# Optimization experiments

Hardware: AMD Instinct MI355X
Metric: run time of the kernel (lower is better)

## Reference

```python
import jax, jax.numpy as jnp
import numpy as np

IMG = 512.0
B, C, A, H, W, M = 16, 3, 9, 128, 128, 32
K = 5 + C
N = A * H * W


def make_anchors():
    # SSD-style anchor grid: 3 scales x 3 aspect ratios per cell on a HxW grid.
    stride = IMG / H
    cx, cy = jnp.meshgrid(
        (jnp.arange(W, dtype=jnp.float32) + 0.5) * stride,
        (jnp.arange(H, dtype=jnp.float32) + 0.5) * stride,
        indexing='xy')
    scales = jnp.array([16.0, 32.0, 64.0], dtype=jnp.float32)
    ratios = jnp.array([0.5, 1.0, 2.0], dtype=jnp.float32)
    ws = (scales[:, None] * jnp.sqrt(ratios)[None, :]).reshape(-1)  # [A]
    hs = (scales[:, None] / jnp.sqrt(ratios)[None, :]).reshape(-1)
    cx = cx[:, :, None]; cy = cy[:, :, None]  # [H,W,1]
    x1 = cx - ws * 0.5; y1 = cy - hs * 0.5
    x2 = cx + ws * 0.5; y2 = cy + hs * 0.5
    anc = jnp.stack([x1, y1, x2, y2], axis=-1)  # [H,W,A,4]
    return anc.reshape(-1, 4)


def setup_inputs() -> dict:
    key = jax.random.key(0)
    k1, k2, k3, k4 = jax.random.split(key, 4)
    pred = jax.random.normal(k1, (B, A * K, H, W), dtype=jnp.float32)
    anchors = make_anchors()  # [N,4]
    xy = jax.random.uniform(k2, (B, M, 2), minval=0.0, maxval=IMG * 0.8)
    wh = jax.random.uniform(k3, (B, M, 2), minval=16.0, maxval=IMG * 0.2)
    gt_boxes = jnp.concatenate([xy, xy + wh], axis=-1).astype(jnp.float32)
    gt_labels = jax.random.randint(k4, (B, M), 1, C + 1).astype(jnp.int32)
    return {'pred': pred, 'anchors': anchors, 'gt_boxes': gt_boxes, 'gt_labels': gt_labels}


def iou_matrix(anc, boxes):
    # anc [N,4], boxes [M,4] -> [N,M]
    lt = jnp.maximum(anc[:, None, :2], boxes[None, :, :2])
    rb = jnp.minimum(anc[:, None, 2:], boxes[None, :, 2:])
    wh = jnp.clip(rb - lt, 0.0)
    inter = wh[..., 0] * wh[..., 1]
    area_a = (anc[:, 2] - anc[:, 0]) * (anc[:, 3] - anc[:, 1])
    area_b = (boxes[:, 2] - boxes[:, 0]) * (boxes[:, 3] - boxes[:, 1])
    union = area_a[:, None] + area_b[None, :] - inter
    return inter / jnp.maximum(union, 1e-9)


def encode_boxes(anc, boxes):
    ax = (anc[..., 0] + anc[..., 2]) * 0.5
    ay = (anc[..., 1] + anc[..., 3]) * 0.5
    aw = jnp.maximum(anc[..., 2] - anc[..., 0], 1e-6)
    ah = jnp.maximum(anc[..., 3] - anc[..., 1], 1e-6)
    gx = (boxes[..., 0] + boxes[..., 2]) * 0.5
    gy = (boxes[..., 1] + boxes[..., 3]) * 0.5
    gw = jnp.maximum(boxes[..., 2] - boxes[..., 0], 1e-6)
    gh = jnp.maximum(boxes[..., 3] - boxes[..., 1], 1e-6)
    return jnp.stack([(gx - ax) / aw, (gy - ay) / ah,
                      jnp.log(gw / aw), jnp.log(gh / ah)], axis=-1)


def bce_logits(x, t):
    return jnp.maximum(x, 0.0) - x * t + jnp.log1p(jnp.exp(-jnp.abs(x)))


def smooth_l1(d):
    ad = jnp.abs(d)
    return jnp.where(ad < 1.0, 0.5 * d * d, ad - 0.5)


def _detection_loss(pred, anchors, gt_boxes, gt_labels):
    pred = jnp.transpose(pred, (0, 2, 3, 1)).reshape(B, N, K)
    pred_box = pred[..., :4]
    pred_obj = pred[..., 4]
    pred_cls = pred[..., 5:]

    def per_image(pbox, pobj, pcls, gtb, gtl):
        iou = iou_matrix(anchors, gtb)          # [N,M]
        best_iou = jnp.max(iou, axis=1)
        best_idx = jnp.argmax(iou, axis=1)
        pos = best_iou >= 0.5
        neg = best_iou < 0.3
        matched_boxes = gtb[best_idx]           # [N,4]
        matched_labels = gtl[best_idx]          # [N]

        obj_loss = bce_logits(pobj, pos.astype(pobj.dtype))  # [N]

        # hard negative mining on detached loss
        num_pos = jnp.sum(pos)
        num_neg = jnp.sum(neg)
        k = jnp.where(num_pos == 0,
                      jnp.where(num_neg > 0, jnp.maximum(num_neg // 10, 1), 0),
                      jnp.minimum(3 * num_pos, num_neg))
        neg_losses = jnp.where(neg, jax.lax.stop_gradient(obj_loss), -1e9)
        rank = jnp.argsort(jnp.argsort(-neg_losses))  # 0 = largest loss
        sel_neg = neg & (rank < k)
        select = pos | sel_neg
        num_sel = jnp.sum(select)
        obj_sum = jnp.sum(jnp.where(select, obj_loss, 0.0))

        # classification: CE over positives, labels are 1-based
        tgt = jnp.clip(matched_labels - 1, 0, C - 1)
        logp = jax.nn.log_softmax(pcls, axis=-1)
        cls_per = -jnp.take_along_axis(logp, tgt[:, None], axis=1)[:, 0]
        cls_sum = jnp.sum(jnp.where(pos, cls_per, 0.0))

        # localization: smooth L1 over positives
        t = encode_boxes(anchors, matched_boxes)
        loc_per = jnp.sum(smooth_l1(pbox - t), axis=-1)
        loc_sum = jnp.sum(jnp.where(pos, loc_per, 0.0))
        return obj_sum, cls_sum, loc_sum, num_pos, num_sel

    obj_s, cls_s, loc_s, npos, nsel = jax.vmap(per_image)(pred_box, pred_obj, pred_cls, gt_boxes, gt_labels)
    total_pos = jnp.sum(npos)
    total_sel = jnp.sum(nsel)
    denom_pos = jnp.maximum(total_pos, 1).astype(jnp.float32)
    denom_obj = jnp.maximum(total_sel, 1).astype(jnp.float32)
    loss_loc = jnp.sum(loc_s) / denom_pos
    loss_cls = jnp.sum(cls_s) / denom_pos
    loss_obj = jnp.sum(obj_s) / denom_obj
    loss_total = 2.0 * loss_loc + 1.0 * loss_cls + 1.0 * loss_obj
    return jnp.stack([loss_obj, loss_cls, loss_loc, loss_total])


def reference(pred, anchors, gt_boxes, gt_labels):
    return _detection_loss(pred, anchors, gt_boxes, gt_labels)
```

## Files before the change

kernel.cpp:

```cpp
#include <hip/hip_runtime.h>

#define BB 16
#define CC 3
#define AA 9
#define MM 32
#define KK 8
#define HWSZ 16384
#define NN (AA*HWSZ)

#define STATS_STRIDE 32
#define ST_NPOS 0
#define ST_NNEG 1
#define ST_OBJP 2
#define ST_CLS  3
#define ST_LOC  4
#define ST_K    5
#define ST_TOPK 6

#define KEYS16_WORDS ((size_t)BB*NN/2)
#define STATS_WORDS (BB*STATS_STRIDE)
#define HIST0_WORDS (BB*512)
#define H1_WORDS    (BB*256)
#define CNT_WORDS   4
#define ZERO_WORDS  (STATS_WORDS + HIST0_WORDS + H1_WORDS + CNT_WORDS)

#define HBLK 16

__device__ __forceinline__ unsigned calc_k(unsigned np, unsigned nn) {
  if (np == 0u) return (nn > 0u) ? ((nn/10u > 1u) ? nn/10u : 1u) : 0u;
  return (3u*np < nn) ? 3u*np : nn;
}

__device__ __forceinline__ void sel1(unsigned lc, float ls, unsigned r,
                                     unsigned* s_c, float* s_s,
                                     unsigned* s_u, float* s_f,
                                     unsigned& bin_out, unsigned& r_out, float& sab_out)
{
  const int t = threadIdx.x;
  s_c[t] = lc; s_s[t] = ls;
  __syncthreads();
  for (int off = 1; off < 256; off <<= 1) {
    unsigned ac = s_c[t]; float as = s_s[t];
    unsigned bc = 0; float bs = 0.f;
    if (t + off < 256) { bc = s_c[t + off]; bs = s_s[t + off]; }
    __syncthreads();
    s_c[t] = ac + bc; s_s[t] = as + bs;
    __syncthreads();
  }
  bool win = (t == 255) ? (s_c[255] >= r) : (s_c[t] >= r && s_c[t+1] < r);
  if (win) {
    unsigned cum = (t < 255) ? s_c[t+1] : 0u;
    float sab = (t < 255) ? s_s[t+1] : 0.f;
    s_u[0] = (unsigned)t; s_u[1] = r - cum; s_f[0] = sab;
  }
  __syncthreads();
  bin_out = s_u[0]; r_out = s_u[1]; sab_out = s_f[0];
  __syncthreads();
}

__global__ __launch_bounds__(256) void k_zero(uint4* __restrict__ p)
{
  const unsigned i = blockIdx.x * 256u + threadIdx.x;
  if (i < ZERO_WORDS/4) p[i] = make_uint4(0u,0u,0u,0u);
}

__global__ __launch_bounds__(256, 4) void k_main(
    const float* __restrict__ pred,
    const float* __restrict__ gtb, const int* __restrict__ gtl,
    unsigned short* __restrict__ keys16, unsigned* __restrict__ stats,
    unsigned* __restrict__ hist0)
{
  __shared__ float4 s_box[MM];
  __shared__ float s_area[MM], s_gx[MM], s_gy[MM], s_gw[MM], s_gh[MM];
  __shared__ int s_lab[MM];
  __shared__ int s_list[MM];
  __shared__ int s_cnt;
  __shared__ unsigned s_hc[8][257];
  __shared__ float s_hs[8][257];
  __shared__ unsigned s_ri[2];
  __shared__ float s_rf[3];
  __shared__ unsigned s_plist[AA*256];
  __shared__ unsigned s_pcnt;

  const int tid = threadIdx.x;
  const int b = blockIdx.x >> 6;
  const int t6 = blockIdx.x & 63;
  const int tr = t6 >> 3, tc = t6 & 7;
  const int hrow = tr*16 + (tid >> 4);
  const int wcol = tc*16 + (tid & 15);
  const int hw = hrow*128 + wcol;

  for (int i = tid; i < 8*257; i += 256) { (&s_hc[0][0])[i] = 0u; (&s_hs[0][0])[i] = 0.f; }
  if (tid == 0) { s_ri[0] = 0u; s_ri[1] = 0u; s_pcnt = 0u; }
  if (tid < 3) s_rf[tid] = 0.f;
  if (tid < MM) {
    float x1 = gtb[((size_t)b*MM + tid)*4 + 0];
    float y1 = gtb[((size_t)b*MM + tid)*4 + 1];
    float x2 = gtb[((size_t)b*MM + tid)*4 + 2];
    float y2 = gtb[((size_t)b*MM + tid)*4 + 3];
    s_box[tid] = make_float4(x1, y1, x2, y2);
    s_area[tid] = (x2 - x1) * (y2 - y1);
    s_gx[tid] = (x1 + x2) * 0.5f;
    s_gy[tid] = (y1 + y2) * 0.5f;
    s_gw[tid] = fmaxf(x2 - x1, 1e-6f);
    s_gh[tid] = fmaxf(y2 - y1, 1e-6f);
    s_lab[tid] = gtl[(size_t)b*MM + tid];
  }
  __syncthreads();

  if (tid < 64) {
    const float cxlo = (float)(tc*64 + 2), cxhi = cxlo + 60.f;
    const float cylo = (float)(tr*64 + 2), cyhi = cylo + 60.f;
    bool keep = false;
    if (tid < MM) {
      float4 bx = s_box[tid];
      keep = (bx.z >= cxlo - 46.f) && (bx.x <= cxhi + 46.f) &&
             (bx.w >= cylo - 46.f) && (bx.y <= cyhi + 46.f);
    }
    unsigned long long mask = __ballot(keep);
    if (keep) s_list[__popcll(mask & ((1ull << tid) - 1ull))] = tid;
    if (tid == 0) s_cnt = (int)__popcll(mask);
  }
  __syncthreads();

  const float cx = ((float)wcol + 0.5f) * 4.0f;
  const float cy = ((float)hrow + 0.5f) * 4.0f;
  float AX1[AA], AY1[AA], AX2[AA], AY2[AA], AREA[AA];
  {
    const float S0[3] = {16.f, 32.f, 64.f};
    const float Q0[3] = {0.70710678118654752440f, 1.0f, 1.41421356237309504880f};
#pragma unroll
    for (int i = 0; i < 3; ++i)
#pragma unroll
      for (int jj = 0; jj < 3; ++jj) {
        int a = i*3 + jj;
        float w2 = S0[i] * Q0[jj] * 0.5f;
        float h2 = (S0[i] / Q0[jj]) * 0.5f;
        float x1 = cx - w2, x2 = cx + w2;
        float y1 = cy - h2, y2 = cy + h2;
        AX1[a]=x1; AX2[a]=x2; AY1[a]=y1; AY2[a]=y2;
        AREA[a] = (x2 - x1) * (y2 - y1);
      }
  }

  float bnum[AA], bden[AA]; int bi[AA];
#pragma unroll
  for (int a = 0; a < AA; ++a) { bnum[a] = 0.f; bden[a] = 1.f; bi[a] = 0; }

  const int cnt = s_cnt;
  for (int jj = 0; jj < cnt; ++jj) {
    const int j = s_list[jj];
    const float4 bx = s_box[j];
    const float ba = s_area[j];
#pragma unroll
    for (int a = 0; a < AA; ++a) {
      float lx = fmaxf(AX1[a], bx.x);
      float ly = fmaxf(AY1[a], bx.y);
      float rx = fminf(AX2[a], bx.z);
      float ry = fminf(AY2[a], bx.w);
      float wx = fmaxf(rx - lx, 0.f);
      float wy = fmaxf(ry - ly, 0.f);
      float inter = wx * wy;
      float den = (AREA[a] + ba) - inter;
      bool bt = inter * bden[a] > bnum[a] * den;
      bnum[a] = bt ? inter : bnum[a];
      bden[a] = bt ? den : bden[a];
      bi[a]   = bt ? j : bi[a];
    }
  }

  const float* pb = pred + (size_t)b * (AA*KK) * HWSZ + hw;
  unsigned short* kout = keys16 + ((size_t)b * AA) * HWSZ + (t6 << 8) + tid;

  const int rep = tid & 7;
  unsigned npos = 0, nneg = 0;
  float objp = 0.f;

#pragma unroll
  for (int a = 0; a < AA; ++a) {
    float best_iou = bnum[a] / bden[a];
    bool pos = best_iou >= 0.5f;
    bool neg = best_iou < 0.3f;

    float x = pb[(size_t)((a*KK + 4) * HWSZ)];
    float e = __expf(-fabsf(x));
    float ol = fmaxf(x, 0.f) - (pos ? x : 0.f) + __logf(1.f + e);

    unsigned key = 0u;
    if (neg) {
      key = __float_as_uint(ol);
      ++nneg;
      atomicAdd(&s_hc[rep][key >> 24], 1u);
      atomicAdd(&s_hs[rep][key >> 24], ol);
    }
    kout[(size_t)a * HWSZ] = (unsigned short)(key >> 16);

    if (pos) {
      ++npos;
      objp += ol;
      unsigned idx = atomicAdd(&s_pcnt, 1u);
      s_plist[idx] = (unsigned)hw | ((unsigned)a << 14) | ((unsigned)bi[a] << 18);
    }
  }

  __syncthreads();

  float cls2 = 0.f, loc2 = 0.f;
  {
    const int pcnt = (int)s_pcnt;
    const float* pball = pred + (size_t)b * (AA*KK) * HWSZ;
    for (int i = tid; i < pcnt; i += 256) {
      unsigned it = s_plist[i];
      int hw2 = (int)(it & 16383u);
      int a2  = (int)((it >> 14) & 15u);
      int jb  = (int)(it >> 18);
      int w2c = hw2 & 127, h2r = hw2 >> 7;
      float cx2 = ((float)w2c + 0.5f) * 4.0f;
      float cy2 = ((float)h2r + 0.5f) * 4.0f;
      int si = a2 / 3, rj = a2 - si*3;
      float s0 = (si == 0) ? 16.f : ((si == 1) ? 32.f : 64.f);
      float q0 = (rj == 0) ? 0.70710678118654752440f : ((rj == 1) ? 1.0f : 1.41421356237309504880f);
      float w2 = s0 * q0 * 0.5f;
      float h2 = (s0 / q0) * 0.5f;
      float ax1 = cx2 - w2, ax2 = cx2 + w2;
      float ay1 = cy2 - h2, ay2 = cy2 + h2;

      const float* pp = pball + hw2;
      float c0 = pp[(size_t)((a2*KK + 5) * HWSZ)];
      float c1 = pp[(size_t)((a2*KK + 6) * HWSZ)];
      float c2 = pp[(size_t)((a2*KK + 7) * HWSZ)];
      int lab = s_lab[jb];
      int tgt = lab - 1; tgt = tgt < 0 ? 0 : (tgt > CC-1 ? CC-1 : tgt);
      float m = fmaxf(fmaxf(c0, c1), c2);
      float lse = m + __logf(__expf(c0-m) + __expf(c1-m) + __expf(c2-m));
      float ct = (tgt == 0) ? c0 : ((tgt == 1) ? c1 : c2);
      cls2 += lse - ct;

      float axc = (ax1 + ax2) * 0.5f;
      float ayc = (ay1 + ay2) * 0.5f;
      float aw = fmaxf(ax2 - ax1, 1e-6f);
      float ah = fmaxf(ay2 - ay1, 1e-6f);
      float t0 = (s_gx[jb] - axc) / aw;
      float t1 = (s_gy[jb] - ayc) / ah;
      float t2 = __logf(s_gw[jb] / aw);
      float t3 = __logf(s_gh[jb] / ah);
      float p0 = pp[(size_t)((a2*KK + 0) * HWSZ)];
      float p1 = pp[(size_t)((a2*KK + 1) * HWSZ)];
      float p2 = pp[(size_t)((a2*KK + 2) * HWSZ)];
      float p3 = pp[(size_t)((a2*KK + 3) * HWSZ)];
      float l = 0.f, d, ad;
      d = p0-t0; ad = fabsf(d); l += (ad < 1.f) ? 0.5f*d*d : ad - 0.5f;
      d = p1-t1; ad = fabsf(d); l += (ad < 1.f) ? 0.5f*d*d : ad - 0.5f;
      d = p2-t2; ad = fabsf(d); l += (ad < 1.f) ? 0.5f*d*d : ad - 0.5f;
      d = p3-t3; ad = fabsf(d); l += (ad < 1.f) ? 0.5f*d*d : ad - 0.5f;
      loc2 += l;
    }
  }

#pragma unroll
  for (int off = 32; off; off >>= 1) {
    npos += __shfl_down(npos, off);
    nneg += __shfl_down(nneg, off);
    objp += __shfl_down(objp, off);
    cls2 += __shfl_down(cls2, off);
    loc2 += __shfl_down(loc2, off);
  }
  if ((tid & 63) == 0) {
    atomicAdd(&s_ri[0], npos);
    atomicAdd(&s_ri[1], nneg);
    atomicAdd(&s_rf[0], objp);
    atomicAdd(&s_rf[1], cls2);
    atomicAdd(&s_rf[2], loc2);
  }
  __syncthreads();

  unsigned* st = stats + b * STATS_STRIDE;
  if (tid == 0) { atomicAdd(&st[ST_NPOS], s_ri[0]); atomicAdd(&st[ST_NNEG], s_ri[1]); }
  else if (tid == 1) atomicAdd((float*)(st + ST_OBJP), s_rf[0]);
  else if (tid == 2) atomicAdd((float*)(st + ST_CLS), s_rf[1]);
  else if (tid == 3) atomicAdd((float*)(st + ST_LOC), s_rf[2]);

  unsigned c = 0; float s = 0.f;
#pragma unroll
  for (int r = 0; r < 8; ++r) { c += s_hc[r][tid]; s += s_hs[r][tid]; }
  if (c) {
    atomicAdd(&hist0[b*512 + tid], c);
    atomicAdd((float*)(hist0 + b*512 + 256 + tid), s);
  }
}

__global__ __launch_bounds__(256) void k_h1(
    const unsigned short* __restrict__ keys16, const unsigned* __restrict__ stats,
    const unsigned* __restrict__ hist0, unsigned* __restrict__ h1)
{
  __shared__ unsigned s_c[256]; __shared__ float s_s[256];
  __shared__ unsigned s_u[2];   __shared__ float s_f[1];
  __shared__ unsigned s_hc[8][257];
  const int tid = threadIdx.x;
  const int b = blockIdx.x >> 4;
  const unsigned* st = stats + b * STATS_STRIDE;
  const unsigned k = calc_k(st[ST_NPOS], st[ST_NNEG]);
  if (k == 0u) return;

  unsigned bin0, r0; float sab;
  sel1(hist0[b*512 + tid], __uint_as_float(hist0[b*512 + 256 + tid]), k,
       s_c, s_s, s_u, s_f, bin0, r0, sab);

  for (int i = tid; i < 8*257; i += 256) (&s_hc[0][0])[i] = 0u;
  __syncthreads();

  const int rep = tid & 7;
  const uint2* kp = (const uint2*)(keys16 + (size_t)b * NN) +
                    (size_t)(blockIdx.x & 15) * 2304;
#pragma unroll
  for (int j = 0; j < 9; ++j) {
    uint2 v = kp[j*256 + tid];
    unsigned k0 = v.x & 0xFFFFu, k1 = v.x >> 16;
    unsigned k2 = v.y & 0xFFFFu, k3 = v.y >> 16;
    if ((k0 >> 8) == bin0) atomicAdd(&s_hc[rep][k0 & 255u], 1u);
    if ((k1 >> 8) == bin0) atomicAdd(&s_hc[rep][k1 & 255u], 1u);
    if ((k2 >> 8) == bin0) atomicAdd(&s_hc[rep][k2 & 255u], 1u);
    if ((k3 >> 8) == bin0) atomicAdd(&s_hc[rep][k3 & 255u], 1u);
  }
  __syncthreads();

  unsigned c = 0;
#pragma unroll
  for (int r = 0; r < 8; ++r) c += s_hc[r][tid];
  if (c) atomicAdd(&h1[b*256 + tid], c);
}

__global__ __launch_bounds__(256) void k_fin(
    const unsigned* __restrict__ hist0, const unsigned* __restrict__ h1,
    unsigned* __restrict__ stats, unsigned* __restrict__ counter,
    float* __restrict__ out)
{
  __shared__ unsigned s_c[256]; __shared__ float s_s[256];
  __shared__ unsigned s_u[2];   __shared__ float s_f[1];
  __shared__ unsigned s_prev;
  const int b = blockIdx.x;
  const int tid = threadIdx.x;
  unsigned* st = stats + b * STATS_STRIDE;
  const unsigned k = calc_k(st[ST_NPOS], st[ST_NNEG]);
  float topk = 0.f;
  if (k) {
    unsigned bin0, r0, bin1, r1;
    float sab0, sab1;
    sel1(hist0[b*512 + tid], __uint_as_float(hist0[b*512 + 256 + tid]), k,
         s_c, s_s, s_u, s_f, bin0, r0, sab0);
    unsigned c1 = h1[b*256 + tid];
    float mid = __uint_as_float((bin0 << 24) | ((unsigned)tid << 16) | 0x8000u);
    sel1(c1, (float)c1 * mid, r0, s_c, s_s, s_u, s_f, bin1, r1, sab1);
    float mid1 = __uint_as_float((bin0 << 24) | (bin1 << 16) | 0x8000u);
    topk = sab0 + sab1 + (float)r1 * mid1;
  }
  if (tid == 0) {
    __hip_atomic_store(&st[ST_K], k, __ATOMIC_RELAXED, __HIP_MEMORY_SCOPE_AGENT);
    __hip_atomic_store((float*)&st[ST_TOPK], topk, __ATOMIC_RELAXED, __HIP_MEMORY_SCOPE_AGENT);
    __threadfence();
    s_prev = __hip_atomic_fetch_add(counter, 1u, __ATOMIC_ACQ_REL, __HIP_MEMORY_SCOPE_AGENT);
  }
  __syncthreads();

  if (s_prev == (unsigned)(BB - 1) && tid < 64) {
    unsigned np = 0, kk = 0;
    float obj = 0.f, cls = 0.f, loc = 0.f;
    if (tid < BB) {
      unsigned* s2 = stats + tid * STATS_STRIDE;
      np  = s2[ST_NPOS];
      cls = ((const float*)s2)[ST_CLS];
      loc = ((const float*)s2)[ST_LOC];
      obj = ((const float*)s2)[ST_OBJP];
      kk  = __hip_atomic_load(&s2[ST_K], __ATOMIC_RELAXED, __HIP_MEMORY_SCOPE_AGENT);
      float tk;
      __hip_atomic_load_n:;
      tk = __hip_atomic_load((float*)&s2[ST_TOPK], __ATOMIC_ACQUIRE, __HIP_MEMORY_SCOPE_AGENT);
      obj += tk;
    }
#pragma unroll
    for (int off = 8; off; off >>= 1) {
      np  += __shfl_down(np, off);
      kk  += __shfl_down(kk, off);
      obj += __shfl_down(obj, off);
      cls += __shfl_down(cls, off);
      loc += __shfl_down(loc, off);
    }
    if (tid == 0) {
      unsigned ts = np + kk;
      float dp  = (float)(np > 1u ? np : 1u);
      float dob = (float)(ts > 1u ? ts : 1u);
      float lo = obj / dob, lc = cls / dp, ll = loc / dp;
      out[0] = lo;
      out[1] = lc;
      out[2] = ll;
      out[3] = 2.f*ll + lc + lo;
    }
  }
}

extern "C" void kernel_launch(void* const* d_in, const int* in_sizes, int n_in,
                              void* d_out, int out_size, void* d_ws, size_t ws_size,
                              hipStream_t stream)
{
  const float* pred = (const float*)d_in[0];
  const float* gtb  = (const float*)d_in[2];
  const int*   gtl  = (const int*)d_in[3];
  float* out = (float*)d_out;

  unsigned* ws    = (unsigned*)d_ws;
  unsigned short* keys16 = (unsigned short*)ws;
  unsigned* stats = ws + KEYS16_WORDS;
  unsigned* hist0 = stats + STATS_WORDS;
  unsigned* h1    = hist0 + HIST0_WORDS;
  unsigned* cnt   = h1 + H1_WORDS;

  k_zero<<<(ZERO_WORDS/4 + 255)/256, 256, 0, stream>>>((uint4*)stats);
  k_main<<<BB*64, 256, 0, stream>>>(pred, gtb, gtl, keys16, stats, hist0);
  k_h1<<<BB*HBLK, 256, 0, stream>>>(keys16, stats, hist0, h1);
  k_fin<<<BB, 256, 0, stream>>>(hist0, h1, stats, cnt, out);
}
```

Measured before the change: 45.87 us.

## Pack negative histogram count and fixed-point sum into one 64-bit atomic

Replaces the separate per-bin count and float-sum shared histograms with one 64-bit word per bin: the count sits in the top 20 bits and a 2^-20 fixed-point loss sum in the low 44 bits, so each negative anchor needs one LDS atomic instead of two, and the global merge is also a single atomic. The objectness logits are now loaded before the IoU loop so their latency overlaps the matching math, and the IoU divisions are replaced by threshold comparisons scaled by the denominator. In exchange, the bin sums are quantised to fixed point, so the top-k sum loses some precision, and the sum field can overflow if a bin gets very large.

```diff
diff --git a/kernel.cpp b/kernel.cpp
--- a/kernel.cpp
+++ b/kernel.cpp
@@ -1,4 +1,6 @@
 #include <hip/hip_runtime.h>
+
+typedef unsigned long long u64;
 
 #define BB 16
 #define CC 3
@@ -25,6 +27,8 @@
 #define ZERO_WORDS  (STATS_WORDS + HIST0_WORDS + H1_WORDS + CNT_WORDS)
 
 #define HBLK 16
+#define SUMMASK ((1ull<<44) - 1ull)
+#define ONECNT  (1ull<<44)
 
 __device__ __forceinline__ unsigned calc_k(unsigned np, unsigned nn) {
   if (np == 0u) return (nn > 0u) ? ((nn/10u > 1u) ? nn/10u : 1u) : 0u;
@@ -68,15 +72,14 @@
     const float* __restrict__ pred,
     const float* __restrict__ gtb, const int* __restrict__ gtl,
     unsigned short* __restrict__ keys16, unsigned* __restrict__ stats,
-    unsigned* __restrict__ hist0)
+    u64* __restrict__ hist0)
 {
   __shared__ float4 s_box[MM];
   __shared__ float s_area[MM], s_gx[MM], s_gy[MM], s_gw[MM], s_gh[MM];
   __shared__ int s_lab[MM];
   __shared__ int s_list[MM];
   __shared__ int s_cnt;
-  __shared__ unsigned s_hc[8][257];
-  __shared__ float s_hs[8][257];
+  __shared__ u64 s_h64[8][257];
   __shared__ unsigned s_ri[2];
   __shared__ float s_rf[3];
   __shared__ unsigned s_plist[AA*256];
@@ -90,7 +93,7 @@
   const int wcol = tc*16 + (tid & 15);
   const int hw = hrow*128 + wcol;
 
-  for (int i = tid; i < 8*257; i += 256) { (&s_hc[0][0])[i] = 0u; (&s_hs[0][0])[i] = 0.f; }
+  for (int i = tid; i < 8*257; i += 256) (&s_h64[0][0])[i] = 0ull;
   if (tid == 0) { s_ri[0] = 0u; s_ri[1] = 0u; s_pcnt = 0u; }
   if (tid < 3) s_rf[tid] = 0.f;
   if (tid < MM) {
@@ -123,6 +126,11 @@
   }
   __syncthreads();
 
+  const float* pb = pred + (size_t)b * (AA*KK) * HWSZ + hw;
+  float xo[AA];
+#pragma unroll
+  for (int a = 0; a < AA; ++a) xo[a] = pb[(size_t)((a*KK + 4) * HWSZ)];
+
   const float cx = ((float)wcol + 0.5f) * 4.0f;
   const float cy = ((float)hrow + 0.5f) * 4.0f;
   float AX1[AA], AY1[AA], AX2[AA], AY2[AA], AREA[AA];
@@ -169,7 +177,6 @@
     }
   }
 
-  const float* pb = pred + (size_t)b * (AA*KK) * HWSZ + hw;
   unsigned short* kout = keys16 + ((size_t)b * AA) * HWSZ + (t6 << 8) + tid;
 
   const int rep = tid & 7;
@@ -178,11 +185,10 @@
 
 #pragma unroll
   for (int a = 0; a < AA; ++a) {
-    float best_iou = bnum[a] / bden[a];
-    bool pos = best_iou >= 0.5f;
-    bool neg = best_iou < 0.3f;
-
-    float x = pb[(size_t)((a*KK + 4) * HWSZ)];
+    bool pos = bnum[a] >= 0.5f * bden[a];
+    bool neg = bnum[a] < 0.3f * bden[a];
+
+    float x = xo[a];
     float e = __expf(-fabsf(x));
     float ol = fmaxf(x, 0.f) - (pos ? x : 0.f) + __logf(1.f + e);
 
@@ -190,8 +196,7 @@
     if (neg) {
       key = __float_as_uint(ol);
       ++nneg;
-      atomicAdd(&s_hc[rep][key >> 24], 1u);
-      atomicAdd(&s_hs[rep][key >> 24], ol);
+      atomicAdd(&s_h64[rep][key >> 24], ONECNT | (u64)(ol * 1048576.0f + 0.5f));
     }
     kout[(size_t)a * HWSZ] = (unsigned short)(key >> 16);
 
@@ -280,18 +285,15 @@
   else if (tid == 2) atomicAdd((float*)(st + ST_CLS), s_rf[1]);
   else if (tid == 3) atomicAdd((float*)(st + ST_LOC), s_rf[2]);
 
-  unsigned c = 0; float s = 0.f;
-#pragma unroll
-  for (int r = 0; r < 8; ++r) { c += s_hc[r][tid]; s += s_hs[r][tid]; }
-  if (c) {
-    atomicAdd(&hist0[b*512 + tid], c);
-    atomicAdd((float*)(hist0 + b*512 + 256 + tid), s);
-  }
+  u64 m = 0ull;
+#pragma unroll
+  for (int r = 0; r < 8; ++r) m += s_h64[r][tid];
+  if (m) atomicAdd(&hist0[b*256 + tid], m);
 }
 
 __global__ __launch_bounds__(256) void k_h1(
     const unsigned short* __restrict__ keys16, const unsigned* __restrict__ stats,
-    const unsigned* __restrict__ hist0, unsigned* __restrict__ h1)
+    const u64* __restrict__ hist0, unsigned* __restrict__ h1)
 {
   __shared__ unsigned s_c[256]; __shared__ float s_s[256];
   __shared__ unsigned s_u[2];   __shared__ float s_f[1];
@@ -303,8 +305,11 @@
   if (k == 0u) return;
 
   unsigned bin0, r0; float sab;
-  sel1(hist0[b*512 + tid], __uint_as_float(hist0[b*512 + 256 + tid]), k,
-       s_c, s_s, s_u, s_f, bin0, r0, sab);
+  {
+    u64 v = hist0[b*256 + tid];
+    sel1((unsigned)(v >> 44), (float)(v & SUMMASK) * 0x1p-20f, k,
+         s_c, s_s, s_u, s_f, bin0, r0, sab);
+  }
 
   for (int i = tid; i < 8*257; i += 256) (&s_hc[0][0])[i] = 0u;
   __syncthreads();
@@ -331,7 +336,7 @@
 }
 
 __global__ __launch_bounds__(256) void k_fin(
-    const unsigned* __restrict__ hist0, const unsigned* __restrict__ h1,
+    const u64* __restrict__ hist0, const unsigned* __restrict__ h1,
     unsigned* __restrict__ stats, unsigned* __restrict__ counter,
     float* __restrict__ out)
 {
@@ -346,8 +351,11 @@
   if (k) {
     unsigned bin0, r0, bin1, r1;
     float sab0, sab1;
-    sel1(hist0[b*512 + tid], __uint_as_float(hist0[b*512 + 256 + tid]), k,
-         s_c, s_s, s_u, s_f, bin0, r0, sab0);
+    {
+      u64 v = hist0[b*256 + tid];
+      sel1((unsigned)(v >> 44), (float)(v & SUMMASK) * 0x1p-20f, k,
+           s_c, s_s, s_u, s_f, bin0, r0, sab0);
+    }
     unsigned c1 = h1[b*256 + tid];
     float mid = __uint_as_float((bin0 << 24) | ((unsigned)tid << 16) | 0x8000u);
     sel1(c1, (float)c1 * mid, r0, s_c, s_s, s_u, s_f, bin1, r1, sab1);
@@ -372,9 +380,7 @@
       loc = ((const float*)s2)[ST_LOC];
       obj = ((const float*)s2)[ST_OBJP];
       kk  = __hip_atomic_load(&s2[ST_K], __ATOMIC_RELAXED, __HIP_MEMORY_SCOPE_AGENT);
-      float tk;
-      __hip_atomic_load_n:;
-      tk = __hip_atomic_load((float*)&s2[ST_TOPK], __ATOMIC_ACQUIRE, __HIP_MEMORY_SCOPE_AGENT);
+      float tk = __hip_atomic_load((float*)&s2[ST_TOPK], __ATOMIC_ACQUIRE, __HIP_MEMORY_SCOPE_AGENT);
       obj += tk;
     }
 #pragma unroll
@@ -410,8 +416,8 @@
   unsigned* ws    = (unsigned*)d_ws;
   unsigned short* keys16 = (unsigned short*)ws;
   unsigned* stats = ws + KEYS16_WORDS;
-  unsigned* hist0 = stats + STATS_WORDS;
-  unsigned* h1    = hist0 + HIST0_WORDS;
+  u64* hist0      = (u64*)(stats + STATS_WORDS);
+  unsigned* h1    = (unsigned*)(hist0 + BB*256);
   unsigned* cnt   = h1 + H1_WORDS;
 
   k_zero<<<(ZERO_WORDS/4 + 255)/256, 256, 0, stream>>>((uint4*)stats);
```

Result: faster. 37.96 us (median of 3 runs) (-17.2%).
